# Optimization experiments

Measured on AMD Instinct MI355X. Metric: run time of the kernel, lower is better.

## Reference

```python
import jax, jax.numpy as jnp
import numpy as np

H = W = 32
V = 1.5  # gaussian sigma used by the original _gussin(1.5)

def _gaussian_table():
    # gus[p, x, y] with p = i*32 + k, matching the original nested loops.
    r = np.arange(H, dtype=np.float64)
    d = (r[:, None, None, None] - r[None, None, :, None]) ** 2 \
        + (r[None, :, None, None] - r[None, None, None, :]) ** 2  # [i,k,x,y]
    g = np.exp(-d / (2.0 * V * V)) / (2.0 * np.pi * V * V)
    g = g.reshape(H * W, H, W)
    g = g / g.sum(axis=(1, 2), keepdims=True)  # per-position boundary normalization
    return jnp.asarray(g, dtype=jnp.float32)

_GUS = _gaussian_table()  # [1024, 32, 32]

def setup_inputs() -> dict:
    key = jax.random.key(0)
    ks = jax.random.split(key, 5)
    c, r = 1024, 16
    return {
        "x": jax.random.normal(ks[0], (1, c, H, W), jnp.float32),
        "se_w1": jax.random.normal(ks[1], (c // r, c), jnp.float32) * 0.03,
        "se_b1": jnp.zeros((c // r,), jnp.float32),
        "se_w2": jax.random.normal(ks[2], (c, c // r), jnp.float32) * 0.1,
        "se_b2": jnp.zeros((c,), jnp.float32),
        "conv_w": jax.random.normal(ks[3], (c, 2 * c), jnp.float32) * 0.02,
        "bn_gamma": jnp.ones((c,), jnp.float32),
        "bn_beta": jnp.zeros((c,), jnp.float32),
        "bn_mean": jnp.zeros((c,), jnp.float32),
        "bn_var": jnp.ones((c,), jnp.float32),
    }

def reference(x, se_w1, se_b1, se_w2, se_b2, conv_w, bn_gamma, bn_beta, bn_mean, bn_var):
    b, c, h, w = x.shape  # b == 1, h == w == 32 (hardcoded by the gaussian table)
    # ---- SE block ----
    y = x.mean(axis=(2, 3))                              # [b, c]
    y = jax.nn.relu(y @ se_w1.T + se_b1)                 # [b, c//r]
    y = jax.nn.sigmoid(y @ se_w2.T + se_b2)              # [b, c]
    x = x * y[:, :, None, None]
    # ---- gaussian spatial pooling (algebraic form of the O(H^2 W^2 C) expand) ----
    # x_spatial[c, p] = sum_{h,w} x[c,h,w] * gus[p,h,w]
    x_spatial = jnp.einsum('chw,phw->cp', x[0], _GUS).reshape(c, h, w)
    # ---- 3x3 local softmax attention on sigmoid features ----
    xr = jax.nn.sigmoid(x)                               # [1, c, h, w]
    xp = jnp.pad(xr, ((0, 0), (0, 0), (1, 1), (1, 1)))
    # torch F.unfold ordering: feature index = c_idx*9 + kh*3 + kw
    patches = jnp.stack([xp[:, :, i:i + h, j:j + w]
                         for i in range(3) for j in range(3)], axis=2)  # [1, c, 9, h, w]
    u = patches.reshape(c * 9, h * w).T                  # [hw, c*9]
    # faithful to the original reshape(hw, 3, 3, c) (reinterprets the c*9 layout)
    x3 = u.reshape(h * w, 3, 3, c)
    x1 = xr[0].transpose(1, 2, 0).reshape(h * w, 1, 1, c)
    logits = (x1 * x3).sum(-1).reshape(h * w, 9)         # [hw, 9]
    attn = jax.nn.softmax(logits, axis=1).reshape(h * w, 3, 3)
    x_range = jnp.einsum('pij,pijc->cp', attn, x3).reshape(c, h, w)
    # ---- fuse: 1x1 conv (no bias) + eval-mode BatchNorm + ReLU ----
    cat = jnp.concatenate([x_range, x_spatial], axis=0).reshape(b, 2 * c, h, w)
    out = jnp.einsum('oc,bchw->bohw', conv_w, cat)
    inv = jax.lax.rsqrt(bn_var + 1e-5)
    out = (out - bn_mean[None, :, None, None]) * (inv * bn_gamma)[None, :, None, None] \
          + bn_beta[None, :, None, None]
    return jax.nn.relu(out)
```

## Files before the change

### kernel.cpp

```cpp
#include <hip/hip_runtime.h>
#include <hip/hip_bf16.h>


typedef __attribute__((ext_vector_type(8))) short v8s;
typedef __attribute__((ext_vector_type(4))) float v4f;

__device__ __forceinline__ float sigmoidf_(float v) {
    return 1.f / (1.f + __expf(-v));
}
__device__ __forceinline__ unsigned short f2bf(float f) {
    unsigned u = __float_as_uint(f);
    u += 0x7fffu + ((u >> 16) & 1u);
    return (unsigned short)(u >> 16);
}
__device__ __forceinline__ float bf2f(unsigned short s) {
    return __uint_as_float(((unsigned)s) << 16);
}

__global__ __launch_bounds__(256) void k_meanW(const float* __restrict__ x,
                                               const float* __restrict__ W,
                                               float* __restrict__ mean,
                                               unsigned short* __restrict__ Wb) {
    int c = blockIdx.x;
    int tid = threadIdx.x;
    size_t e0 = (size_t)c * 2048 + (size_t)tid * 8;
    float4 v0 = *(const float4*)(W + e0);
    float4 v1 = *(const float4*)(W + e0 + 4);
    uint4 pk;
    pk.x = (unsigned)f2bf(v0.x) | ((unsigned)f2bf(v0.y) << 16);
    pk.y = (unsigned)f2bf(v0.z) | ((unsigned)f2bf(v0.w) << 16);
    pk.z = (unsigned)f2bf(v1.x) | ((unsigned)f2bf(v1.y) << 16);
    pk.w = (unsigned)f2bf(v1.z) | ((unsigned)f2bf(v1.w) << 16);
    *(uint4*)(Wb + e0) = pk;
    const float* xp = x + (size_t)c * 1024;
    float s = xp[tid] + xp[tid + 256] + xp[tid + 512] + xp[tid + 768];
    #pragma unroll
    for (int o = 32; o; o >>= 1) s += __shfl_down(s, o);
    __shared__ float wsum[4];
    if ((tid & 63) == 0) wsum[tid >> 6] = s;
    __syncthreads();
    if (tid == 0) mean[c] = (wsum[0] + wsum[1] + wsum[2] + wsum[3]) * (1.f / 1024.f);
}

__global__ __launch_bounds__(1024) void k_se(const float* __restrict__ mean,
                                             const float* __restrict__ w1,
                                             const float* __restrict__ b1,
                                             const float* __restrict__ w2,
                                             const float* __restrict__ b2,
                                             float* __restrict__ y2) {
    __shared__ float ms[1024];
    __shared__ float y1[64];
    __shared__ float w2t[64 * 65];
    int tid = threadIdx.x;
    int c0 = blockIdx.x << 6;
    ms[tid] = mean[tid];
    #pragma unroll
    for (int i = 0; i < 4; ++i) {
        int idx = tid + (i << 10);
        w2t[(idx >> 6) * 65 + (idx & 63)] = w2[(size_t)c0 * 64 + idx];
    }
    __syncthreads();
    int wv = tid >> 6, lane = tid & 63;
    #pragma unroll
    for (int jj = 0; jj < 4; ++jj) {
        int j = (wv << 2) + jj;
        float s = 0.f;
        #pragma unroll
        for (int kk = 0; kk < 4; ++kk) {
            float4 wv4 = *(const float4*)(w1 + (size_t)j * 1024 + kk * 256 + (lane << 2));
            float4 mv  = *(const float4*)&ms[kk * 256 + (lane << 2)];
            s += wv4.x * mv.x + wv4.y * mv.y + wv4.z * mv.z + wv4.w * mv.w;
        }
        #pragma unroll
        for (int o = 32; o; o >>= 1) s += __shfl_down(s, o);
        if (lane == 0) y1[j] = fmaxf(s + b1[j], 0.f);
    }
    __syncthreads();
    int o = tid >> 4, l = tid & 15;
    float s = 0.f;
    #pragma unroll
    for (int jj = 0; jj < 4; ++jj) s += y1[l + (jj << 4)] * w2t[o * 65 + l + (jj << 4)];
    #pragma unroll
    for (int o2 = 8; o2; o2 >>= 1) s += __shfl_down(s, o2, 16);
    if (l == 0) y2[c0 + o] = sigmoidf_(s + b2[c0 + o]);
}

__global__ __launch_bounds__(256) void k_prep(const float* __restrict__ x,
                                              const float* __restrict__ y2,
                                              unsigned short* __restrict__ Xsb,
                                              unsigned short* __restrict__ xrb) {
    __shared__ float T[64][65];
    int tid = threadIdx.x;
    int p0 = blockIdx.x << 6, c0 = blockIdx.y << 6;
    #pragma unroll
    for (int i = 0; i < 4; ++i) {
        int idx = tid + (i << 8);
        int row = idx >> 4;
        int col = (idx & 15) << 2;
        float sc = y2[c0 + row];
        float4 v = *(const float4*)(x + (size_t)(c0 + row) * 1024 + p0 + col);
        uint2 pk;
        pk.x = (unsigned)f2bf(v.x * sc) | ((unsigned)f2bf(v.y * sc) << 16);
        pk.y = (unsigned)f2bf(v.z * sc) | ((unsigned)f2bf(v.w * sc) << 16);
        *(uint2*)(Xsb + (size_t)(c0 + row) * 1024 + p0 + col) = pk;
        T[col + 0][row] = sigmoidf_(v.x * sc);
        T[col + 1][row] = sigmoidf_(v.y * sc);
        T[col + 2][row] = sigmoidf_(v.z * sc);
        T[col + 3][row] = sigmoidf_(v.w * sc);
    }
    __syncthreads();
    #pragma unroll
    for (int i = 0; i < 4; ++i) {
        int idx = tid + (i << 8);
        int prow = idx >> 4;
        int cc = (idx & 15) << 2;
        uint2 pk;
        pk.x = (unsigned)f2bf(T[prow][cc + 0]) | ((unsigned)f2bf(T[prow][cc + 1]) << 16);
        pk.y = (unsigned)f2bf(T[prow][cc + 2]) | ((unsigned)f2bf(T[prow][cc + 3]) << 16);
        *(uint2*)(xrb + (size_t)(p0 + prow) * 1024 + c0 + cc) = pk;
    }
}

union SMem {
    struct { unsigned short As[64 * 72]; unsigned short Bs[64 * 72]; float Gs[32][32]; } sp;
    struct { unsigned short val[9216]; float part[9][4]; } at;
};

__global__ __launch_bounds__(256) void k_spattn(const unsigned short* __restrict__ Xsb,
                                                const unsigned short* __restrict__ xrb,
                                                unsigned short* __restrict__ Bt) {
    __shared__ SMem sm;
    int tid = threadIdx.x;
    int bx = blockIdx.x;
    if (bx < 256) {
        {
            int row = tid >> 3, col0 = (tid & 7) << 2;
            float e[4], s = 0.f;
            #pragma unroll
            for (int j = 0; j < 4; ++j) {
                float d = (float)(row - (col0 + j));
                e[j] = __expf(-d * d / 4.5f);
                s += e[j];
            }
            s += __shfl_xor(s, 4, 8);
            s += __shfl_xor(s, 2, 8);
            s += __shfl_xor(s, 1, 8);
            float is = 1.f / s;
            #pragma unroll
            for (int j = 0; j < 4; ++j) sm.sp.Gs[row][col0 + j] = e[j] * is;
        }
        int wv = tid >> 6, lane = tid & 63;
        int wm = wv & 1, wn = wv >> 1;
        int m0 = (bx >> 4) << 6, n0 = (bx & 15) << 6;
        int col = lane & 15, quad = lane >> 4;
        int smi = tid >> 2;
        int sg = (tid & 3) * 2;
        int pm = m0 + smi;
        int rr = pm >> 5, qq = pm & 31;
        v4f acc[2][2];
        #pragma unroll
        for (int i = 0; i < 2; ++i)
            #pragma unroll
            for (int j = 0; j < 2; ++j) acc[i][j] = (v4f){0.f, 0.f, 0.f, 0.f};
        const float4* pb = (const float4*)(Xsb + (size_t)(n0 + smi) * 1024 + sg * 8);
        float4 rb0 = pb[0], rb1 = pb[1];
        for (int it = 0; it < 16; ++it) {
            __syncthreads();
            int k0 = it << 6;
            unsigned pk[8];
            #pragma unroll
            for (int jj = 0; jj < 8; ++jj) {
                int hw0 = k0 + sg * 8 + jj * 2;
                float v0 = sm.sp.Gs[rr][hw0 >> 5] * sm.sp.Gs[qq][hw0 & 31];
                float v1 = sm.sp.Gs[rr][(hw0 + 1) >> 5] * sm.sp.Gs[qq][(hw0 + 1) & 31];
                pk[jj] = (unsigned)f2bf(v0) | ((unsigned)f2bf(v1) << 16);
            }
            *(uint2*)&sm.sp.As[smi * 72 + sg * 8]      = *(uint2*)&pk[0];
            *(uint2*)&sm.sp.As[smi * 72 + sg * 8 + 4]  = *(uint2*)&pk[2];
            *(uint2*)&sm.sp.As[smi * 72 + sg * 8 + 8]  = *(uint2*)&pk[4];
            *(uint2*)&sm.sp.As[smi * 72 + sg * 8 + 12] = *(uint2*)&pk[6];
            *(float4*)&sm.sp.Bs[smi * 72 + sg * 8] = rb0;
            *(float4*)&sm.sp.Bs[smi * 72 + sg * 8 + 8] = rb1;
            __syncthreads();
            if (it + 1 < 16) {
                pb = (const float4*)(Xsb + (size_t)(n0 + smi) * 1024 + ((it + 1) << 6) + sg * 8);
                rb0 = pb[0]; rb1 = pb[1];
            }
            #pragma unroll
            for (int ks = 0; ks < 2; ++ks) {
                int kg = ks * 4 + quad;
                int rA = wm * 32 + col;
                int rB = wn * 32 + col;
                v8s a0 = *(const v8s*)&sm.sp.As[rA * 72 + kg * 8];
                v8s a1 = *(const v8s*)&sm.sp.As[(rA + 16) * 72 + kg * 8];
                v8s b0 = *(const v8s*)&sm.sp.Bs[rB * 72 + kg * 8];
                v8s b1 = *(const v8s*)&sm.sp.Bs[(rB + 16) * 72 + kg * 8];
                acc[0][0] = __builtin_amdgcn_mfma_f32_16x16x32_bf16(a0, b0, acc[0][0], 0, 0, 0);
                acc[0][1] = __builtin_amdgcn_mfma_f32_16x16x32_bf16(a0, b1, acc[0][1], 0, 0, 0);
                acc[1][0] = __builtin_amdgcn_mfma_f32_16x16x32_bf16(a1, b0, acc[1][0], 0, 0, 0);
                acc[1][1] = __builtin_amdgcn_mfma_f32_16x16x32_bf16(a1, b1, acc[1][1], 0, 0, 0);
            }
        }
        #pragma unroll
        for (int mi = 0; mi < 2; ++mi)
            #pragma unroll
            for (int ni = 0; ni < 2; ++ni) {
                int mb = m0 + wm * 32 + mi * 16 + quad * 4;
                int nn = n0 + wn * 32 + ni * 16 + col;
                #pragma unroll
                for (int r = 0; r < 4; ++r)
                    Bt[(size_t)(mb + r) * 2048 + 1024 + nn] = f2bf(acc[mi][ni][r]);
            }
    } else {
        int p = bx - 256;
        int h = p >> 5, w = p & 31;
        int wv = tid >> 6, lane = tid & 63;
        #pragma unroll
        for (int rem = 0; rem < 9; ++rem) {
            int dh = rem / 3 - 1, dw = rem % 3 - 1;
            bool ok = ((unsigned)(h + dh) < 32u) && ((unsigned)(w + dw) < 32u);
            const unsigned short* rp = xrb + (size_t)((h + dh) * 32 + (w + dw)) * 1024;
            #pragma unroll
            for (int j = 0; j < 4; ++j) {
                int cf = tid + (j << 8);
                sm.at.val[cf * 9 + rem] = ok ? rp[cf] : (unsigned short)0;
            }
        }
        __syncthreads();
        float ctr[4], vv[9][4], lg[9];
        #pragma unroll
        for (int j = 0; j < 4; ++j) ctr[j] = bf2f(sm.at.val[(4 * tid + j) * 9 + 4]);
        #pragma unroll
        for (int q = 0; q < 9; ++q) {
            uint2 pk = *(const uint2*)&sm.at.val[q * 1024 + 4 * tid];
            vv[q][0] = bf2f((unsigned short)(pk.x & 0xffffu));
            vv[q][1] = bf2f((unsigned short)(pk.x >> 16));
            vv[q][2] = bf2f((unsigned short)(pk.y & 0xffffu));
            vv[q][3] = bf2f((unsigned short)(pk.y >> 16));
            lg[q] = ctr[0] * vv[q][0] + ctr[1] * vv[q][1]
                  + ctr[2] * vv[q][2] + ctr[3] * vv[q][3];
        }
        #pragma unroll
        for (int q = 0; q < 9; ++q) {
            float s = lg[q];
            #pragma unroll
            for (int o = 32; o; o >>= 1) s += __shfl_down(s, o);
            if (lane == 0) sm.at.part[q][wv] = s;
        }
        __syncthreads();
        float a9[9], mx = -3.4e38f;
        #pragma unroll
        for (int q = 0; q < 9; ++q) {
            a9[q] = sm.at.part[q][0] + sm.at.part[q][1] + sm.at.part[q][2] + sm.at.part[q][3];
            mx = fmaxf(mx, a9[q]);
        }
        float se = 0.f;
        #pragma unroll
        for (int q = 0; q < 9; ++q) { a9[q] = __expf(a9[q] - mx); se += a9[q]; }
        float inv = 1.f / se;
        float o4[4] = {0.f, 0.f, 0.f, 0.f};
        #pragma unroll
        for (int q = 0; q < 9; ++q) {
            float a = a9[q] * inv;
            #pragma unroll
            for (int j = 0; j < 4; ++j) o4[j] += a * vv[q][j];
        }
        uint2 pk;
        pk.x = (unsigned)f2bf(o4[0]) | ((unsigned)f2bf(o4[1]) << 16);
        pk.y = (unsigned)f2bf(o4[2]) | ((unsigned)f2bf(o4[3]) << 16);
        *(uint2*)(Bt + (size_t)p * 2048 + 4 * tid) = pk;
    }
}

__global__ __launch_bounds__(256) void k_gemm_main(
    const unsigned short* __restrict__ A, const unsigned short* __restrict__ B,
    float* __restrict__ outF,
    const float* __restrict__ gamma, const float* __restrict__ beta,
    const float* __restrict__ mu, const float* __restrict__ var) {
    __shared__ unsigned short As[64 * 72];
    __shared__ unsigned short Bs[64 * 72];
    const int K = 2048;
    int tid = threadIdx.x;
    int wv = tid >> 6, lane = tid & 63;
    int wm = wv & 1, wn = wv >> 1;
    int m0 = blockIdx.y << 6, n0 = blockIdx.x << 6;
    int col = lane & 15, quad = lane >> 4;
    int sm = tid >> 2;
    int sg = (tid & 3) * 2;
    v4f acc[2][2];
    #pragma unroll
    for (int i = 0; i < 2; ++i)
        #pragma unroll
        for (int j = 0; j < 2; ++j) acc[i][j] = (v4f){0.f, 0.f, 0.f, 0.f};

    const float4* pa = (const float4*)(A + (size_t)(m0 + sm) * K + sg * 8);
    const float4* pb = (const float4*)(B + (size_t)(n0 + sm) * K + sg * 8);
    float4 ra0 = pa[0], ra1 = pa[1], rb0 = pb[0], rb1 = pb[1];
    for (int it = 0; it < 32; ++it) {
        __syncthreads();
        *(float4*)&As[sm * 72 + sg * 8] = ra0;
        *(float4*)&As[sm * 72 + sg * 8 + 8] = ra1;
        *(float4*)&Bs[sm * 72 + sg * 8] = rb0;
        *(float4*)&Bs[sm * 72 + sg * 8 + 8] = rb1;
        __syncthreads();
        if (it + 1 < 32) {
            int k0 = (it + 1) << 6;
            pa = (const float4*)(A + (size_t)(m0 + sm) * K + k0 + sg * 8);
            pb = (const float4*)(B + (size_t)(n0 + sm) * K + k0 + sg * 8);
            ra0 = pa[0]; ra1 = pa[1];
            rb0 = pb[0]; rb1 = pb[1];
        }
        #pragma unroll
        for (int ks = 0; ks < 2; ++ks) {
            int kg = ks * 4 + quad;
            int rA = wm * 32 + col;
            int rB = wn * 32 + col;
            v8s a0 = *(const v8s*)&As[rA * 72 + kg * 8];
            v8s a1 = *(const v8s*)&As[(rA + 16) * 72 + kg * 8];
            v8s b0 = *(const v8s*)&Bs[rB * 72 + kg * 8];
            v8s b1 = *(const v8s*)&Bs[(rB + 16) * 72 + kg * 8];
            acc[0][0] = __builtin_amdgcn_mfma_f32_16x16x32_bf16(a0, b0, acc[0][0], 0, 0, 0);
            acc[0][1] = __builtin_amdgcn_mfma_f32_16x16x32_bf16(a0, b1, acc[0][1], 0, 0, 0);
            acc[1][0] = __builtin_amdgcn_mfma_f32_16x16x32_bf16(a1, b0, acc[1][0], 0, 0, 0);
            acc[1][1] = __builtin_amdgcn_mfma_f32_16x16x32_bf16(a1, b1, acc[1][1], 0, 0, 0);
        }
    }
    #pragma unroll
    for (int mi = 0; mi < 2; ++mi)
        #pragma unroll
        for (int ni = 0; ni < 2; ++ni) {
            int mb = m0 + wm * 32 + mi * 16 + quad * 4;
            int nn = n0 + wn * 32 + ni * 16 + col;
            #pragma unroll
            for (int r = 0; r < 4; ++r) {
                int mm = mb + r;
                float iv = rsqrtf(var[mm] + 1e-5f);
                float sc = iv * gamma[mm];
                float sh = beta[mm] - mu[mm] * sc;
                outF[((size_t)mm << 10) + nn] = fmaxf(fmaf(acc[mi][ni][r], sc, sh), 0.f);
            }
        }
}

extern "C" void kernel_launch(void* const* d_in, const int* in_sizes, int n_in,
                              void* d_out, int out_size, void* d_ws, size_t ws_size,
                              hipStream_t stream) {
    const float* x     = (const float*)d_in[0];
    const float* w1    = (const float*)d_in[1];
    const float* b1    = (const float*)d_in[2];
    const float* w2    = (const float*)d_in[3];
    const float* b2    = (const float*)d_in[4];
    const float* cw    = (const float*)d_in[5];
    const float* gamma = (const float*)d_in[6];
    const float* beta  = (const float*)d_in[7];
    const float* mu    = (const float*)d_in[8];
    const float* var   = (const float*)d_in[9];
    float* wsf = (float*)d_ws;
    unsigned short* Wb  = (unsigned short*)wsf;
    unsigned short* Bt  = (unsigned short*)(wsf + (1 << 20));
    unsigned short* Xsb = (unsigned short*)(wsf + (2 << 20));
    unsigned short* xrb = (unsigned short*)(wsf + (2 << 20) + (1 << 19));
    float* mean = wsf + (3 << 20);
    float* y2   = mean + 1024;
    float* out  = (float*)d_out;

    dim3 g16(16, 16);
    k_meanW    <<<1024, 256, 0, stream>>>(x, cw, mean, Wb);
    k_se       <<<16, 1024, 0, stream>>>(mean, w1, b1, w2, b2, y2);
    k_prep     <<<g16, 256, 0, stream>>>(x, y2, Xsb, xrb);
    k_spattn   <<<1280, 256, 0, stream>>>(Xsb, xrb, Bt);
    k_gemm_main<<<g16, 256, 0, stream>>>(Wb, Bt, out, gamma, beta, mu, var);
}
```

Baseline: 134.7 us.

## Fuse all stages into one cooperative persistent kernel with grid syncs

Merges the five separate launches (mean/weight-convert, SE, prep, spatial+attention, final GEMM) into a single cooperative kernel of 256 blocks separated by grid.sync barriers. Each block handles 4 channel means and 4 attention positions, and the fp32 conv weight is converted to bf16 inside the GEMM load loop instead of a separate pass. The aim is to remove kernel launch gaps and the Wb write/read round trip. The cost is much less parallelism in some phases: SE runs on only 16 blocks, attention on 256 blocks looping 4 times, and every phase waits on grid-wide barriers.

```diff
diff --git a/kernel.cpp b/kernel.cpp
--- a/kernel.cpp
+++ b/kernel.cpp
@@ -1,5 +1,8 @@
 #include <hip/hip_runtime.h>
 #include <hip/hip_bf16.h>
+#include <hip/hip_cooperative_groups.h>
+
+namespace cg = cooperative_groups;
 
 
 typedef __attribute__((ext_vector_type(8))) short v8s;
@@ -17,122 +20,114 @@
     return __uint_as_float(((unsigned)s) << 16);
 }
 
-__global__ __launch_bounds__(256) void k_meanW(const float* __restrict__ x,
-                                               const float* __restrict__ W,
-                                               float* __restrict__ mean,
-                                               unsigned short* __restrict__ Wb) {
-    int c = blockIdx.x;
-    int tid = threadIdx.x;
-    size_t e0 = (size_t)c * 2048 + (size_t)tid * 8;
-    float4 v0 = *(const float4*)(W + e0);
-    float4 v1 = *(const float4*)(W + e0 + 4);
-    uint4 pk;
-    pk.x = (unsigned)f2bf(v0.x) | ((unsigned)f2bf(v0.y) << 16);
-    pk.y = (unsigned)f2bf(v0.z) | ((unsigned)f2bf(v0.w) << 16);
-    pk.z = (unsigned)f2bf(v1.x) | ((unsigned)f2bf(v1.y) << 16);
-    pk.w = (unsigned)f2bf(v1.z) | ((unsigned)f2bf(v1.w) << 16);
-    *(uint4*)(Wb + e0) = pk;
-    const float* xp = x + (size_t)c * 1024;
-    float s = xp[tid] + xp[tid + 256] + xp[tid + 512] + xp[tid + 768];
-    #pragma unroll
-    for (int o = 32; o; o >>= 1) s += __shfl_down(s, o);
-    __shared__ float wsum[4];
-    if ((tid & 63) == 0) wsum[tid >> 6] = s;
-    __syncthreads();
-    if (tid == 0) mean[c] = (wsum[0] + wsum[1] + wsum[2] + wsum[3]) * (1.f / 1024.f);
-}
-
-__global__ __launch_bounds__(1024) void k_se(const float* __restrict__ mean,
-                                             const float* __restrict__ w1,
-                                             const float* __restrict__ b1,
-                                             const float* __restrict__ w2,
-                                             const float* __restrict__ b2,
-                                             float* __restrict__ y2) {
-    __shared__ float ms[1024];
-    __shared__ float y1[64];
-    __shared__ float w2t[64 * 65];
-    int tid = threadIdx.x;
-    int c0 = blockIdx.x << 6;
-    ms[tid] = mean[tid];
-    #pragma unroll
-    for (int i = 0; i < 4; ++i) {
-        int idx = tid + (i << 10);
-        w2t[(idx >> 6) * 65 + (idx & 63)] = w2[(size_t)c0 * 64 + idx];
-    }
-    __syncthreads();
-    int wv = tid >> 6, lane = tid & 63;
-    #pragma unroll
-    for (int jj = 0; jj < 4; ++jj) {
-        int j = (wv << 2) + jj;
-        float s = 0.f;
-        #pragma unroll
-        for (int kk = 0; kk < 4; ++kk) {
-            float4 wv4 = *(const float4*)(w1 + (size_t)j * 1024 + kk * 256 + (lane << 2));
-            float4 mv  = *(const float4*)&ms[kk * 256 + (lane << 2)];
-            s += wv4.x * mv.x + wv4.y * mv.y + wv4.z * mv.z + wv4.w * mv.w;
-        }
-        #pragma unroll
-        for (int o = 32; o; o >>= 1) s += __shfl_down(s, o);
-        if (lane == 0) y1[j] = fmaxf(s + b1[j], 0.f);
-    }
-    __syncthreads();
-    int o = tid >> 4, l = tid & 15;
-    float s = 0.f;
-    #pragma unroll
-    for (int jj = 0; jj < 4; ++jj) s += y1[l + (jj << 4)] * w2t[o * 65 + l + (jj << 4)];
-    #pragma unroll
-    for (int o2 = 8; o2; o2 >>= 1) s += __shfl_down(s, o2, 16);
-    if (l == 0) y2[c0 + o] = sigmoidf_(s + b2[c0 + o]);
-}
-
-__global__ __launch_bounds__(256) void k_prep(const float* __restrict__ x,
-                                              const float* __restrict__ y2,
-                                              unsigned short* __restrict__ Xsb,
-                                              unsigned short* __restrict__ xrb) {
-    __shared__ float T[64][65];
-    int tid = threadIdx.x;
-    int p0 = blockIdx.x << 6, c0 = blockIdx.y << 6;
-    #pragma unroll
-    for (int i = 0; i < 4; ++i) {
-        int idx = tid + (i << 8);
-        int row = idx >> 4;
-        int col = (idx & 15) << 2;
-        float sc = y2[c0 + row];
-        float4 v = *(const float4*)(x + (size_t)(c0 + row) * 1024 + p0 + col);
-        uint2 pk;
-        pk.x = (unsigned)f2bf(v.x * sc) | ((unsigned)f2bf(v.y * sc) << 16);
-        pk.y = (unsigned)f2bf(v.z * sc) | ((unsigned)f2bf(v.w * sc) << 16);
-        *(uint2*)(Xsb + (size_t)(c0 + row) * 1024 + p0 + col) = pk;
-        T[col + 0][row] = sigmoidf_(v.x * sc);
-        T[col + 1][row] = sigmoidf_(v.y * sc);
-        T[col + 2][row] = sigmoidf_(v.z * sc);
-        T[col + 3][row] = sigmoidf_(v.w * sc);
-    }
-    __syncthreads();
-    #pragma unroll
-    for (int i = 0; i < 4; ++i) {
-        int idx = tid + (i << 8);
-        int prow = idx >> 4;
-        int cc = (idx & 15) << 2;
-        uint2 pk;
-        pk.x = (unsigned)f2bf(T[prow][cc + 0]) | ((unsigned)f2bf(T[prow][cc + 1]) << 16);
-        pk.y = (unsigned)f2bf(T[prow][cc + 2]) | ((unsigned)f2bf(T[prow][cc + 3]) << 16);
-        *(uint2*)(xrb + (size_t)(p0 + prow) * 1024 + c0 + cc) = pk;
-    }
-}
-
-union SMem {
-    struct { unsigned short As[64 * 72]; unsigned short Bs[64 * 72]; float Gs[32][32]; } sp;
+union __align__(16) MegaSmem {
+    struct { float ms[1024]; float y1[64]; float w2t[64 * 65]; } se;
+    struct { float T[64][65]; } pr;
+    struct { unsigned short As[64 * 72]; unsigned short Bs[64 * 72];
+             float Gs[32][32]; } sp;
     struct { unsigned short val[9216]; float part[9][4]; } at;
+    struct { unsigned short As[64 * 72]; unsigned short Bs[64 * 72]; } gm;
 };
 
-__global__ __launch_bounds__(256) void k_spattn(const unsigned short* __restrict__ Xsb,
-                                                const unsigned short* __restrict__ xrb,
-                                                unsigned short* __restrict__ Bt) {
-    __shared__ SMem sm;
+__global__ __launch_bounds__(256) void k_mega(
+    const float* __restrict__ x, const float* __restrict__ w1,
+    const float* __restrict__ b1, const float* __restrict__ w2,
+    const float* __restrict__ b2, const float* __restrict__ W,
+    const float* __restrict__ gamma, const float* __restrict__ beta,
+    const float* __restrict__ mu, const float* __restrict__ var,
+    float* __restrict__ mean, float* __restrict__ y2,
+    unsigned short* __restrict__ Xsb, unsigned short* __restrict__ xrb,
+    unsigned short* __restrict__ Bt, float* __restrict__ out) {
+    __shared__ MegaSmem sm;
+    cg::grid_group grid = cg::this_grid();
     int tid = threadIdx.x;
     int bx = blockIdx.x;
-    if (bx < 256) {
+    int wv = tid >> 6, lane = tid & 63;
+
+    {
+        int c = (bx << 2) + wv;
+        const float* xp = x + (size_t)c * 1024;
+        float4 a = *(const float4*)(xp + (lane << 2));
+        float4 b4 = *(const float4*)(xp + 256 + (lane << 2));
+        float4 c4 = *(const float4*)(xp + 512 + (lane << 2));
+        float4 d4 = *(const float4*)(xp + 768 + (lane << 2));
+        float s = a.x + a.y + a.z + a.w + b4.x + b4.y + b4.z + b4.w
+                + c4.x + c4.y + c4.z + c4.w + d4.x + d4.y + d4.z + d4.w;
+        #pragma unroll
+        for (int o = 32; o; o >>= 1) s += __shfl_down(s, o);
+        if (lane == 0) mean[c] = s * (1.f / 1024.f);
+    }
+    __threadfence();
+    grid.sync();
+
+    if (bx < 16) {
+        int c0 = bx << 6;
+        #pragma unroll
+        for (int i = 0; i < 4; ++i) sm.se.ms[tid + (i << 8)] = mean[tid + (i << 8)];
+        #pragma unroll
+        for (int i = 0; i < 16; ++i) {
+            int idx = tid + (i << 8);
+            sm.se.w2t[(idx >> 6) * 65 + (idx & 63)] = w2[(size_t)c0 * 64 + idx];
+        }
+        __syncthreads();
+        for (int jj = 0; jj < 16; ++jj) {
+            int j = wv * 16 + jj;
+            float s = 0.f;
+            #pragma unroll
+            for (int kk = 0; kk < 4; ++kk) {
+                float4 wv4 = *(const float4*)(w1 + (size_t)j * 1024 + kk * 256 + (lane << 2));
+                float4 mv  = *(const float4*)&sm.se.ms[kk * 256 + (lane << 2)];
+                s += wv4.x * mv.x + wv4.y * mv.y + wv4.z * mv.z + wv4.w * mv.w;
+            }
+            #pragma unroll
+            for (int o = 32; o; o >>= 1) s += __shfl_down(s, o);
+            if (lane == 0) sm.se.y1[j] = fmaxf(s + b1[j], 0.f);
+        }
+        __syncthreads();
+        if (tid < 64) {
+            float s = 0.f;
+            #pragma unroll 16
+            for (int jj = 0; jj < 64; ++jj) s += sm.se.y1[jj] * sm.se.w2t[tid * 65 + jj];
+            y2[c0 + tid] = sigmoidf_(s + b2[c0 + tid]);
+        }
+    }
+    __threadfence();
+    grid.sync();
+
+    {
+        int p0 = (bx & 15) << 6, c0 = (bx >> 4) << 6;
+        #pragma unroll
+        for (int i = 0; i < 4; ++i) {
+            int idx = tid + (i << 8);
+            int row = idx >> 4;
+            int col = (idx & 15) << 2;
+            float sc = y2[c0 + row];
+            float4 v = *(const float4*)(x + (size_t)(c0 + row) * 1024 + p0 + col);
+            uint2 pk;
+            pk.x = (unsigned)f2bf(v.x * sc) | ((unsigned)f2bf(v.y * sc) << 16);
+            pk.y = (unsigned)f2bf(v.z * sc) | ((unsigned)f2bf(v.w * sc) << 16);
+            *(uint2*)(Xsb + (size_t)(c0 + row) * 1024 + p0 + col) = pk;
+            sm.pr.T[col + 0][row] = sigmoidf_(v.x * sc);
+            sm.pr.T[col + 1][row] = sigmoidf_(v.y * sc);
+            sm.pr.T[col + 2][row] = sigmoidf_(v.z * sc);
+            sm.pr.T[col + 3][row] = sigmoidf_(v.w * sc);
+        }
+        __syncthreads();
+        #pragma unroll
+        for (int i = 0; i < 4; ++i) {
+            int idx = tid + (i << 8);
+            int prow = idx >> 4;
+            int cc = (idx & 15) << 2;
+            uint2 pk;
+            pk.x = (unsigned)f2bf(sm.pr.T[prow][cc + 0]) | ((unsigned)f2bf(sm.pr.T[prow][cc + 1]) << 16);
+            pk.y = (unsigned)f2bf(sm.pr.T[prow][cc + 2]) | ((unsigned)f2bf(sm.pr.T[prow][cc + 3]) << 16);
+            *(uint2*)(xrb + (size_t)(p0 + prow) * 1024 + c0 + cc) = pk;
+        }
+    }
+    __threadfence();
+    grid.sync();
+
+    {
         {
             int row = tid >> 3, col0 = (tid & 7) << 2;
             float e[4], s = 0.f;
@@ -149,7 +144,6 @@
             #pragma unroll
             for (int j = 0; j < 4; ++j) sm.sp.Gs[row][col0 + j] = e[j] * is;
         }
-        int wv = tid >> 6, lane = tid & 63;
         int wm = wv & 1, wn = wv >> 1;
         int m0 = (bx >> 4) << 6, n0 = (bx & 15) << 6;
         int col = lane & 15, quad = lane >> 4;
@@ -211,10 +205,12 @@
                 for (int r = 0; r < 4; ++r)
                     Bt[(size_t)(mb + r) * 2048 + 1024 + nn] = f2bf(acc[mi][ni][r]);
             }
-    } else {
-        int p = bx - 256;
+    }
+
+    for (int pi = 0; pi < 4; ++pi) {
+        int p = (bx << 2) + pi;
         int h = p >> 5, w = p & 31;
-        int wv = tid >> 6, lane = tid & 63;
+        __syncthreads();
         #pragma unroll
         for (int rem = 0; rem < 9; ++rem) {
             int dh = rem / 3 - 1, dw = rem % 3 - 1;
@@ -227,18 +223,18 @@
             }
         }
         __syncthreads();
-        float ctr[4], vv[9][4], lg[9];
+        float ctr[4], vvq[9][4], lg[9];
         #pragma unroll
         for (int j = 0; j < 4; ++j) ctr[j] = bf2f(sm.at.val[(4 * tid + j) * 9 + 4]);
         #pragma unroll
         for (int q = 0; q < 9; ++q) {
             uint2 pk = *(const uint2*)&sm.at.val[q * 1024 + 4 * tid];
-            vv[q][0] = bf2f((unsigned short)(pk.x & 0xffffu));
-            vv[q][1] = bf2f((unsigned short)(pk.x >> 16));
-            vv[q][2] = bf2f((unsigned short)(pk.y & 0xffffu));
-            vv[q][3] = bf2f((unsigned short)(pk.y >> 16));
-            lg[q] = ctr[0] * vv[q][0] + ctr[1] * vv[q][1]
-                  + ctr[2] * vv[q][2] + ctr[3] * vv[q][3];
+            vvq[q][0] = bf2f((unsigned short)(pk.x & 0xffffu));
+            vvq[q][1] = bf2f((unsigned short)(pk.x >> 16));
+            vvq[q][2] = bf2f((unsigned short)(pk.y & 0xffffu));
+            vvq[q][3] = bf2f((unsigned short)(pk.y >> 16));
+            lg[q] = ctr[0] * vvq[q][0] + ctr[1] * vvq[q][1]
+                  + ctr[2] * vvq[q][2] + ctr[3] * vvq[q][3];
         }
         #pragma unroll
         for (int q = 0; q < 9; ++q) {
@@ -263,83 +259,87 @@
         for (int q = 0; q < 9; ++q) {
             float a = a9[q] * inv;
             #pragma unroll
-            for (int j = 0; j < 4; ++j) o4[j] += a * vv[q][j];
+            for (int j = 0; j < 4; ++j) o4[j] += a * vvq[q][j];
         }
         uint2 pk;
         pk.x = (unsigned)f2bf(o4[0]) | ((unsigned)f2bf(o4[1]) << 16);
         pk.y = (unsigned)f2bf(o4[2]) | ((unsigned)f2bf(o4[3]) << 16);
         *(uint2*)(Bt + (size_t)p * 2048 + 4 * tid) = pk;
     }
-}
-
-__global__ __launch_bounds__(256) void k_gemm_main(
-    const unsigned short* __restrict__ A, const unsigned short* __restrict__ B,
-    float* __restrict__ outF,
-    const float* __restrict__ gamma, const float* __restrict__ beta,
-    const float* __restrict__ mu, const float* __restrict__ var) {
-    __shared__ unsigned short As[64 * 72];
-    __shared__ unsigned short Bs[64 * 72];
-    const int K = 2048;
-    int tid = threadIdx.x;
-    int wv = tid >> 6, lane = tid & 63;
-    int wm = wv & 1, wn = wv >> 1;
-    int m0 = blockIdx.y << 6, n0 = blockIdx.x << 6;
-    int col = lane & 15, quad = lane >> 4;
-    int sm = tid >> 2;
-    int sg = (tid & 3) * 2;
-    v4f acc[2][2];
-    #pragma unroll
-    for (int i = 0; i < 2; ++i)
-        #pragma unroll
-        for (int j = 0; j < 2; ++j) acc[i][j] = (v4f){0.f, 0.f, 0.f, 0.f};
-
-    const float4* pa = (const float4*)(A + (size_t)(m0 + sm) * K + sg * 8);
-    const float4* pb = (const float4*)(B + (size_t)(n0 + sm) * K + sg * 8);
-    float4 ra0 = pa[0], ra1 = pa[1], rb0 = pb[0], rb1 = pb[1];
-    for (int it = 0; it < 32; ++it) {
-        __syncthreads();
-        *(float4*)&As[sm * 72 + sg * 8] = ra0;
-        *(float4*)&As[sm * 72 + sg * 8 + 8] = ra1;
-        *(float4*)&Bs[sm * 72 + sg * 8] = rb0;
-        *(float4*)&Bs[sm * 72 + sg * 8 + 8] = rb1;
-        __syncthreads();
-        if (it + 1 < 32) {
-            int k0 = (it + 1) << 6;
-            pa = (const float4*)(A + (size_t)(m0 + sm) * K + k0 + sg * 8);
-            pb = (const float4*)(B + (size_t)(n0 + sm) * K + k0 + sg * 8);
-            ra0 = pa[0]; ra1 = pa[1];
-            rb0 = pb[0]; rb1 = pb[1];
-        }
-        #pragma unroll
-        for (int ks = 0; ks < 2; ++ks) {
-            int kg = ks * 4 + quad;
-            int rA = wm * 32 + col;
-            int rB = wn * 32 + col;
-            v8s a0 = *(const v8s*)&As[rA * 72 + kg * 8];
-            v8s a1 = *(const v8s*)&As[(rA + 16) * 72 + kg * 8];
-            v8s b0 = *(const v8s*)&Bs[rB * 72 + kg * 8];
-            v8s b1 = *(const v8s*)&Bs[(rB + 16) * 72 + kg * 8];
-            acc[0][0] = __builtin_amdgcn_mfma_f32_16x16x32_bf16(a0, b0, acc[0][0], 0, 0, 0);
-            acc[0][1] = __builtin_amdgcn_mfma_f32_16x16x32_bf16(a0, b1, acc[0][1], 0, 0, 0);
-            acc[1][0] = __builtin_amdgcn_mfma_f32_16x16x32_bf16(a1, b0, acc[1][0], 0, 0, 0);
-            acc[1][1] = __builtin_amdgcn_mfma_f32_16x16x32_bf16(a1, b1, acc[1][1], 0, 0, 0);
-        }
-    }
-    #pragma unroll
-    for (int mi = 0; mi < 2; ++mi)
-        #pragma unroll
-        for (int ni = 0; ni < 2; ++ni) {
-            int mb = m0 + wm * 32 + mi * 16 + quad * 4;
-            int nn = n0 + wn * 32 + ni * 16 + col;
-            #pragma unroll
-            for (int r = 0; r < 4; ++r) {
-                int mm = mb + r;
-                float iv = rsqrtf(var[mm] + 1e-5f);
-                float sc = iv * gamma[mm];
-                float sh = beta[mm] - mu[mm] * sc;
-                outF[((size_t)mm << 10) + nn] = fmaxf(fmaf(acc[mi][ni][r], sc, sh), 0.f);
-            }
-        }
+    __threadfence();
+    grid.sync();
+
+    {
+        int wm = wv & 1, wn = wv >> 1;
+        int m0 = (bx >> 4) << 6, n0 = (bx & 15) << 6;
+        int col = lane & 15, quad = lane >> 4;
+        int smi = tid >> 2;
+        int sg = (tid & 3) * 2;
+        v4f acc[2][2];
+        #pragma unroll
+        for (int i = 0; i < 2; ++i)
+            #pragma unroll
+            for (int j = 0; j < 2; ++j) acc[i][j] = (v4f){0.f, 0.f, 0.f, 0.f};
+        const float* pw = W + (size_t)(m0 + smi) * 2048 + sg * 8;
+        const float4* pb = (const float4*)(Bt + (size_t)(n0 + smi) * 2048 + sg * 8);
+        float4 wa0 = *(const float4*)pw, wa1 = *(const float4*)(pw + 4);
+        float4 wa2 = *(const float4*)(pw + 8), wa3 = *(const float4*)(pw + 12);
+        float4 rb0 = pb[0], rb1 = pb[1];
+        for (int it = 0; it < 32; ++it) {
+            __syncthreads();
+            uint4 pk0, pk1;
+            pk0.x = (unsigned)f2bf(wa0.x) | ((unsigned)f2bf(wa0.y) << 16);
+            pk0.y = (unsigned)f2bf(wa0.z) | ((unsigned)f2bf(wa0.w) << 16);
+            pk0.z = (unsigned)f2bf(wa1.x) | ((unsigned)f2bf(wa1.y) << 16);
+            pk0.w = (unsigned)f2bf(wa1.z) | ((unsigned)f2bf(wa1.w) << 16);
+            pk1.x = (unsigned)f2bf(wa2.x) | ((unsigned)f2bf(wa2.y) << 16);
+            pk1.y = (unsigned)f2bf(wa2.z) | ((unsigned)f2bf(wa2.w) << 16);
+            pk1.z = (unsigned)f2bf(wa3.x) | ((unsigned)f2bf(wa3.y) << 16);
+            pk1.w = (unsigned)f2bf(wa3.z) | ((unsigned)f2bf(wa3.w) << 16);
+            *(uint4*)&sm.gm.As[smi * 72 + sg * 8] = pk0;
+            *(uint4*)&sm.gm.As[smi * 72 + sg * 8 + 8] = pk1;
+            *(float4*)&sm.gm.Bs[smi * 72 + sg * 8] = rb0;
+            *(float4*)&sm.gm.Bs[smi * 72 + sg * 8 + 8] = rb1;
+            __syncthreads();
+            if (it + 1 < 32) {
+                int k0 = (it + 1) << 6;
+                pw = W + (size_t)(m0 + smi) * 2048 + k0 + sg * 8;
+                pb = (const float4*)(Bt + (size_t)(n0 + smi) * 2048 + k0 + sg * 8);
+                wa0 = *(const float4*)pw; wa1 = *(const float4*)(pw + 4);
+                wa2 = *(const float4*)(pw + 8); wa3 = *(const float4*)(pw + 12);
+                rb0 = pb[0]; rb1 = pb[1];
+            }
+            #pragma unroll
+            for (int ks = 0; ks < 2; ++ks) {
+                int kg = ks * 4 + quad;
+                int rA = wm * 32 + col;
+                int rB = wn * 32 + col;
+                v8s a0 = *(const v8s*)&sm.gm.As[rA * 72 + kg * 8];
+                v8s a1 = *(const v8s*)&sm.gm.As[(rA + 16) * 72 + kg * 8];
+                v8s b0 = *(const v8s*)&sm.gm.Bs[rB * 72 + kg * 8];
+                v8s b1 = *(const v8s*)&sm.gm.Bs[(rB + 16) * 72 + kg * 8];
+                acc[0][0] = __builtin_amdgcn_mfma_f32_16x16x32_bf16(a0, b0, acc[0][0], 0, 0, 0);
+                acc[0][1] = __builtin_amdgcn_mfma_f32_16x16x32_bf16(a0, b1, acc[0][1], 0, 0, 0);
+                acc[1][0] = __builtin_amdgcn_mfma_f32_16x16x32_bf16(a1, b0, acc[1][0], 0, 0, 0);
+                acc[1][1] = __builtin_amdgcn_mfma_f32_16x16x32_bf16(a1, b1, acc[1][1], 0, 0, 0);
+            }
+        }
+        #pragma unroll
+        for (int mi = 0; mi < 2; ++mi)
+            #pragma unroll
+            for (int ni = 0; ni < 2; ++ni) {
+                int mb = m0 + wm * 32 + mi * 16 + quad * 4;
+                int nn = n0 + wn * 32 + ni * 16 + col;
+                #pragma unroll
+                for (int r = 0; r < 4; ++r) {
+                    int mm = mb + r;
+                    float iv = rsqrtf(var[mm] + 1e-5f);
+                    float sc = iv * gamma[mm];
+                    float sh = beta[mm] - mu[mm] * sc;
+                    out[((size_t)mm << 10) + nn] = fmaxf(fmaf(acc[mi][ni][r], sc, sh), 0.f);
+                }
+            }
+    }
 }
 
 extern "C" void kernel_launch(void* const* d_in, const int* in_sizes, int n_in,
@@ -356,7 +356,6 @@
     const float* mu    = (const float*)d_in[8];
     const float* var   = (const float*)d_in[9];
     float* wsf = (float*)d_ws;
-    unsigned short* Wb  = (unsigned short*)wsf;
     unsigned short* Bt  = (unsigned short*)(wsf + (1 << 20));
     unsigned short* Xsb = (unsigned short*)(wsf + (2 << 20));
     unsigned short* xrb = (unsigned short*)(wsf + (2 << 20) + (1 << 19));
@@ -364,10 +363,11 @@
     float* y2   = mean + 1024;
     float* out  = (float*)d_out;
 
-    dim3 g16(16, 16);
-    k_meanW    <<<1024, 256, 0, stream>>>(x, cw, mean, Wb);
-    k_se       <<<16, 1024, 0, stream>>>(mean, w1, b1, w2, b2, y2);
-    k_prep     <<<g16, 256, 0, stream>>>(x, y2, Xsb, xrb);
-    k_spattn   <<<1280, 256, 0, stream>>>(Xsb, xrb, Bt);
-    k_gemm_main<<<g16, 256, 0, stream>>>(Wb, Bt, out, gamma, beta, mu, var);
-}
+    void* args[] = {
+        (void*)&x, (void*)&w1, (void*)&b1, (void*)&w2, (void*)&b2, (void*)&cw,
+        (void*)&gamma, (void*)&beta, (void*)&mu, (void*)&var,
+        (void*)&mean, (void*)&y2, (void*)&Xsb, (void*)&xrb, (void*)&Bt, (void*)&out
+    };
+    hipLaunchCooperativeKernel((const void*)k_mega, dim3(256), dim3(256),
+                               args, 0, stream);
+}
```

Result: slower. 348.5 us (+158.8%).

## Eliminate prep kernel by folding SE scale into GEMM epilogue and attention gather

Applied to the files above, without the earlier changes.

Drops the separate k_prep kernel. The first kernel now writes unscaled bf16 x alongside the mean and weight conversion, using fewer, larger blocks. The SE scale is applied after the spatial GEMM by scaling output columns, which is valid because the scale is per channel. The attention branch gathers x directly with strided global reads and computes the sigmoid in place, holding fp32 values in shared memory. The final GEMM also gains a double-buffered LDS, removing one barrier per k-step. The trade-off is uncoalesced strided x reads in the attention path and a larger shared-memory footprint.

```diff
diff --git a/kernel.cpp b/kernel.cpp
--- a/kernel.cpp
+++ b/kernel.cpp
@@ -13,33 +13,39 @@
     u += 0x7fffu + ((u >> 16) & 1u);
     return (unsigned short)(u >> 16);
 }
-__device__ __forceinline__ float bf2f(unsigned short s) {
-    return __uint_as_float(((unsigned)s) << 16);
-}
-
-__global__ __launch_bounds__(256) void k_meanW(const float* __restrict__ x,
-                                               const float* __restrict__ W,
-                                               float* __restrict__ mean,
-                                               unsigned short* __restrict__ Wb) {
-    int c = blockIdx.x;
-    int tid = threadIdx.x;
-    size_t e0 = (size_t)c * 2048 + (size_t)tid * 8;
-    float4 v0 = *(const float4*)(W + e0);
-    float4 v1 = *(const float4*)(W + e0 + 4);
-    uint4 pk;
-    pk.x = (unsigned)f2bf(v0.x) | ((unsigned)f2bf(v0.y) << 16);
-    pk.y = (unsigned)f2bf(v0.z) | ((unsigned)f2bf(v0.w) << 16);
-    pk.z = (unsigned)f2bf(v1.x) | ((unsigned)f2bf(v1.y) << 16);
-    pk.w = (unsigned)f2bf(v1.z) | ((unsigned)f2bf(v1.w) << 16);
-    *(uint4*)(Wb + e0) = pk;
+
+__global__ __launch_bounds__(256) void k_A(const float* __restrict__ x,
+                                           const float* __restrict__ W,
+                                           float* __restrict__ mean,
+                                           unsigned short* __restrict__ xb,
+                                           unsigned short* __restrict__ Wb) {
+    int tid = threadIdx.x, bx = blockIdx.x;
+    int wv = tid >> 6, lane = tid & 63;
+    #pragma unroll
+    for (int k = 0; k < 8; ++k) {
+        int e = (k << 18) + (bx << 10) + (tid << 2);
+        float4 v = *(const float4*)(W + e);
+        uint2 pk;
+        pk.x = (unsigned)f2bf(v.x) | ((unsigned)f2bf(v.y) << 16);
+        pk.y = (unsigned)f2bf(v.z) | ((unsigned)f2bf(v.w) << 16);
+        *(uint2*)(Wb + e) = pk;
+    }
+    int c = (bx << 2) + wv;
     const float* xp = x + (size_t)c * 1024;
-    float s = xp[tid] + xp[tid + 256] + xp[tid + 512] + xp[tid + 768];
+    float s = 0.f;
+    #pragma unroll
+    for (int j = 0; j < 4; ++j) {
+        int o = (j << 8) + (lane << 2);
+        float4 v = *(const float4*)(xp + o);
+        uint2 pk;
+        pk.x = (unsigned)f2bf(v.x) | ((unsigned)f2bf(v.y) << 16);
+        pk.y = (unsigned)f2bf(v.z) | ((unsigned)f2bf(v.w) << 16);
+        *(uint2*)(xb + (size_t)c * 1024 + o) = pk;
+        s += v.x + v.y + v.z + v.w;
+    }
     #pragma unroll
     for (int o = 32; o; o >>= 1) s += __shfl_down(s, o);
-    __shared__ float wsum[4];
-    if ((tid & 63) == 0) wsum[tid >> 6] = s;
-    __syncthreads();
-    if (tid == 0) mean[c] = (wsum[0] + wsum[1] + wsum[2] + wsum[3]) * (1.f / 1024.f);
+    if (lane == 0) mean[c] = s * (1.f / 1024.f);
 }
 
 __global__ __launch_bounds__(1024) void k_se(const float* __restrict__ mean,
@@ -85,53 +91,19 @@
     if (l == 0) y2[c0 + o] = sigmoidf_(s + b2[c0 + o]);
 }
 
-__global__ __launch_bounds__(256) void k_prep(const float* __restrict__ x,
-                                              const float* __restrict__ y2,
-                                              unsigned short* __restrict__ Xsb,
-                                              unsigned short* __restrict__ xrb) {
-    __shared__ float T[64][65];
-    int tid = threadIdx.x;
-    int p0 = blockIdx.x << 6, c0 = blockIdx.y << 6;
-    #pragma unroll
-    for (int i = 0; i < 4; ++i) {
-        int idx = tid + (i << 8);
-        int row = idx >> 4;
-        int col = (idx & 15) << 2;
-        float sc = y2[c0 + row];
-        float4 v = *(const float4*)(x + (size_t)(c0 + row) * 1024 + p0 + col);
-        uint2 pk;
-        pk.x = (unsigned)f2bf(v.x * sc) | ((unsigned)f2bf(v.y * sc) << 16);
-        pk.y = (unsigned)f2bf(v.z * sc) | ((unsigned)f2bf(v.w * sc) << 16);
-        *(uint2*)(Xsb + (size_t)(c0 + row) * 1024 + p0 + col) = pk;
-        T[col + 0][row] = sigmoidf_(v.x * sc);
-        T[col + 1][row] = sigmoidf_(v.y * sc);
-        T[col + 2][row] = sigmoidf_(v.z * sc);
-        T[col + 3][row] = sigmoidf_(v.w * sc);
-    }
-    __syncthreads();
-    #pragma unroll
-    for (int i = 0; i < 4; ++i) {
-        int idx = tid + (i << 8);
-        int prow = idx >> 4;
-        int cc = (idx & 15) << 2;
-        uint2 pk;
-        pk.x = (unsigned)f2bf(T[prow][cc + 0]) | ((unsigned)f2bf(T[prow][cc + 1]) << 16);
-        pk.y = (unsigned)f2bf(T[prow][cc + 2]) | ((unsigned)f2bf(T[prow][cc + 3]) << 16);
-        *(uint2*)(xrb + (size_t)(p0 + prow) * 1024 + c0 + cc) = pk;
-    }
-}
-
-union SMem {
+union __align__(16) SMem {
     struct { unsigned short As[64 * 72]; unsigned short Bs[64 * 72]; float Gs[32][32]; } sp;
-    struct { unsigned short val[9216]; float part[9][4]; } at;
+    struct { float val[9216]; float part[9][4]; } at;
 };
 
-__global__ __launch_bounds__(256) void k_spattn(const unsigned short* __restrict__ Xsb,
-                                                const unsigned short* __restrict__ xrb,
+__global__ __launch_bounds__(256) void k_spattn(const float* __restrict__ x,
+                                                const unsigned short* __restrict__ xb,
+                                                const float* __restrict__ y2,
                                                 unsigned short* __restrict__ Bt) {
     __shared__ SMem sm;
     int tid = threadIdx.x;
     int bx = blockIdx.x;
+    int wv = tid >> 6, lane = tid & 63;
     if (bx < 256) {
         {
             int row = tid >> 3, col0 = (tid & 7) << 2;
@@ -149,7 +121,6 @@
             #pragma unroll
             for (int j = 0; j < 4; ++j) sm.sp.Gs[row][col0 + j] = e[j] * is;
         }
-        int wv = tid >> 6, lane = tid & 63;
         int wm = wv & 1, wn = wv >> 1;
         int m0 = (bx >> 4) << 6, n0 = (bx & 15) << 6;
         int col = lane & 15, quad = lane >> 4;
@@ -162,7 +133,7 @@
         for (int i = 0; i < 2; ++i)
             #pragma unroll
             for (int j = 0; j < 2; ++j) acc[i][j] = (v4f){0.f, 0.f, 0.f, 0.f};
-        const float4* pb = (const float4*)(Xsb + (size_t)(n0 + smi) * 1024 + sg * 8);
+        const float4* pb = (const float4*)(xb + (size_t)(n0 + smi) * 1024 + sg * 8);
         float4 rb0 = pb[0], rb1 = pb[1];
         for (int it = 0; it < 16; ++it) {
             __syncthreads();
@@ -183,7 +154,7 @@
             *(float4*)&sm.sp.Bs[smi * 72 + sg * 8 + 8] = rb1;
             __syncthreads();
             if (it + 1 < 16) {
-                pb = (const float4*)(Xsb + (size_t)(n0 + smi) * 1024 + ((it + 1) << 6) + sg * 8);
+                pb = (const float4*)(xb + (size_t)(n0 + smi) * 1024 + ((it + 1) << 6) + sg * 8);
                 rb0 = pb[0]; rb1 = pb[1];
             }
             #pragma unroll
@@ -207,38 +178,39 @@
             for (int ni = 0; ni < 2; ++ni) {
                 int mb = m0 + wm * 32 + mi * 16 + quad * 4;
                 int nn = n0 + wn * 32 + ni * 16 + col;
+                float yv = y2[nn];
                 #pragma unroll
                 for (int r = 0; r < 4; ++r)
-                    Bt[(size_t)(mb + r) * 2048 + 1024 + nn] = f2bf(acc[mi][ni][r]);
+                    Bt[(size_t)(mb + r) * 2048 + 1024 + nn] = f2bf(acc[mi][ni][r] * yv);
             }
     } else {
         int p = bx - 256;
         int h = p >> 5, w = p & 31;
-        int wv = tid >> 6, lane = tid & 63;
+        float yv[4];
+        #pragma unroll
+        for (int j = 0; j < 4; ++j) yv[j] = y2[tid + (j << 8)];
         #pragma unroll
         for (int rem = 0; rem < 9; ++rem) {
             int dh = rem / 3 - 1, dw = rem % 3 - 1;
             bool ok = ((unsigned)(h + dh) < 32u) && ((unsigned)(w + dw) < 32u);
-            const unsigned short* rp = xrb + (size_t)((h + dh) * 32 + (w + dw)) * 1024;
+            int pp = (h + dh) * 32 + (w + dw);
             #pragma unroll
             for (int j = 0; j < 4; ++j) {
                 int cf = tid + (j << 8);
-                sm.at.val[cf * 9 + rem] = ok ? rp[cf] : (unsigned short)0;
+                float v = 0.f;
+                if (ok) v = sigmoidf_(x[(size_t)cf * 1024 + pp] * yv[j]);
+                sm.at.val[cf * 9 + rem] = v;
             }
         }
         __syncthreads();
-        float ctr[4], vv[9][4], lg[9];
-        #pragma unroll
-        for (int j = 0; j < 4; ++j) ctr[j] = bf2f(sm.at.val[(4 * tid + j) * 9 + 4]);
+        float ctr[4], vvq[9][4], lg[9];
+        #pragma unroll
+        for (int j = 0; j < 4; ++j) ctr[j] = sm.at.val[(4 * tid + j) * 9 + 4];
         #pragma unroll
         for (int q = 0; q < 9; ++q) {
-            uint2 pk = *(const uint2*)&sm.at.val[q * 1024 + 4 * tid];
-            vv[q][0] = bf2f((unsigned short)(pk.x & 0xffffu));
-            vv[q][1] = bf2f((unsigned short)(pk.x >> 16));
-            vv[q][2] = bf2f((unsigned short)(pk.y & 0xffffu));
-            vv[q][3] = bf2f((unsigned short)(pk.y >> 16));
-            lg[q] = ctr[0] * vv[q][0] + ctr[1] * vv[q][1]
-                  + ctr[2] * vv[q][2] + ctr[3] * vv[q][3];
+            float4 v4 = *(const float4*)&sm.at.val[(q << 10) + 4 * tid];
+            vvq[q][0] = v4.x; vvq[q][1] = v4.y; vvq[q][2] = v4.z; vvq[q][3] = v4.w;
+            lg[q] = ctr[0] * v4.x + ctr[1] * v4.y + ctr[2] * v4.z + ctr[3] * v4.w;
         }
         #pragma unroll
         for (int q = 0; q < 9; ++q) {
@@ -263,7 +235,7 @@
         for (int q = 0; q < 9; ++q) {
             float a = a9[q] * inv;
             #pragma unroll
-            for (int j = 0; j < 4; ++j) o4[j] += a * vv[q][j];
+            for (int j = 0; j < 4; ++j) o4[j] += a * vvq[q][j];
         }
         uint2 pk;
         pk.x = (unsigned)f2bf(o4[0]) | ((unsigned)f2bf(o4[1]) << 16);
@@ -272,13 +244,13 @@
     }
 }
 
-__global__ __launch_bounds__(256) void k_gemm_main(
+__global__ __launch_bounds__(256) void k_main(
     const unsigned short* __restrict__ A, const unsigned short* __restrict__ B,
     float* __restrict__ outF,
     const float* __restrict__ gamma, const float* __restrict__ beta,
     const float* __restrict__ mu, const float* __restrict__ var) {
-    __shared__ unsigned short As[64 * 72];
-    __shared__ unsigned short Bs[64 * 72];
+    __shared__ unsigned short As[2][64 * 72];
+    __shared__ unsigned short Bs[2][64 * 72];
     const int K = 2048;
     int tid = threadIdx.x;
     int wv = tid >> 6, lane = tid & 63;
@@ -296,13 +268,13 @@
     const float4* pa = (const float4*)(A + (size_t)(m0 + sm) * K + sg * 8);
     const float4* pb = (const float4*)(B + (size_t)(n0 + sm) * K + sg * 8);
     float4 ra0 = pa[0], ra1 = pa[1], rb0 = pb[0], rb1 = pb[1];
+    *(float4*)&As[0][sm * 72 + sg * 8] = ra0;
+    *(float4*)&As[0][sm * 72 + sg * 8 + 8] = ra1;
+    *(float4*)&Bs[0][sm * 72 + sg * 8] = rb0;
+    *(float4*)&Bs[0][sm * 72 + sg * 8 + 8] = rb1;
     for (int it = 0; it < 32; ++it) {
         __syncthreads();
-        *(float4*)&As[sm * 72 + sg * 8] = ra0;
-        *(float4*)&As[sm * 72 + sg * 8 + 8] = ra1;
-        *(float4*)&Bs[sm * 72 + sg * 8] = rb0;
-        *(float4*)&Bs[sm * 72 + sg * 8 + 8] = rb1;
-        __syncthreads();
+        int cur = it & 1;
         if (it + 1 < 32) {
             int k0 = (it + 1) << 6;
             pa = (const float4*)(A + (size_t)(m0 + sm) * K + k0 + sg * 8);
@@ -315,14 +287,21 @@
             int kg = ks * 4 + quad;
             int rA = wm * 32 + col;
             int rB = wn * 32 + col;
-            v8s a0 = *(const v8s*)&As[rA * 72 + kg * 8];
-            v8s a1 = *(const v8s*)&As[(rA + 16) * 72 + kg * 8];
-            v8s b0 = *(const v8s*)&Bs[rB * 72 + kg * 8];
-            v8s b1 = *(const v8s*)&Bs[(rB + 16) * 72 + kg * 8];
+            v8s a0 = *(const v8s*)&As[cur][rA * 72 + kg * 8];
+            v8s a1 = *(const v8s*)&As[cur][(rA + 16) * 72 + kg * 8];
+            v8s b0 = *(const v8s*)&Bs[cur][rB * 72 + kg * 8];
+            v8s b1 = *(const v8s*)&Bs[cur][(rB + 16) * 72 + kg * 8];
             acc[0][0] = __builtin_amdgcn_mfma_f32_16x16x32_bf16(a0, b0, acc[0][0], 0, 0, 0);
             acc[0][1] = __builtin_amdgcn_mfma_f32_16x16x32_bf16(a0, b1, acc[0][1], 0, 0, 0);
             acc[1][0] = __builtin_amdgcn_mfma_f32_16x16x32_bf16(a1, b0, acc[1][0], 0, 0, 0);
             acc[1][1] = __builtin_amdgcn_mfma_f32_16x16x32_bf16(a1, b1, acc[1][1], 0, 0, 0);
+        }
+        if (it + 1 < 32) {
+            int nxt = cur ^ 1;
+            *(float4*)&As[nxt][sm * 72 + sg * 8] = ra0;
+            *(float4*)&As[nxt][sm * 72 + sg * 8 + 8] = ra1;
+            *(float4*)&Bs[nxt][sm * 72 + sg * 8] = rb0;
+            *(float4*)&Bs[nxt][sm * 72 + sg * 8 + 8] = rb1;
         }
     }
     #pragma unroll
@@ -356,18 +335,16 @@
     const float* mu    = (const float*)d_in[8];
     const float* var   = (const float*)d_in[9];
     float* wsf = (float*)d_ws;
-    unsigned short* Wb  = (unsigned short*)wsf;
-    unsigned short* Bt  = (unsigned short*)(wsf + (1 << 20));
-    unsigned short* Xsb = (unsigned short*)(wsf + (2 << 20));
-    unsigned short* xrb = (unsigned short*)(wsf + (2 << 20) + (1 << 19));
+    unsigned short* Wb = (unsigned short*)wsf;
+    unsigned short* Bt = (unsigned short*)(wsf + (1 << 20));
+    unsigned short* xb = (unsigned short*)(wsf + (2 << 20));
     float* mean = wsf + (3 << 20);
     float* y2   = mean + 1024;
     float* out  = (float*)d_out;
 
     dim3 g16(16, 16);
-    k_meanW    <<<1024, 256, 0, stream>>>(x, cw, mean, Wb);
-    k_se       <<<16, 1024, 0, stream>>>(mean, w1, b1, w2, b2, y2);
-    k_prep     <<<g16, 256, 0, stream>>>(x, y2, Xsb, xrb);
-    k_spattn   <<<1280, 256, 0, stream>>>(Xsb, xrb, Bt);
-    k_gemm_main<<<g16, 256, 0, stream>>>(Wb, Bt, out, gamma, beta, mu, var);
-}
+    k_A     <<<256, 256, 0, stream>>>(x, cw, mean, xb, Wb);
+    k_se    <<<16, 1024, 0, stream>>>(mean, w1, b1, w2, b2, y2);
+    k_spattn<<<1280, 256, 0, stream>>>(x, xb, y2, Bt);
+    k_main  <<<g16, 256, 0, stream>>>(Wb, Bt, out, gamma, beta, mu, var);
+}
```

Measured after the change: 159.3 us. +18.2%, slower.
